# Kernel tuning notes

Hardware: AMD Instinct MI355X
Metric: run time of the kernel (lower is better)

## Reference

```python
import jax, jax.numpy as jnp
import numpy as np

GREEDY_EPS = 1e-6

def setup_inputs() -> dict:
    key = jax.random.key(0)
    k1, k2, k3 = jax.random.split(key, 3)
    B, V = 256, 128000
    logits = jax.random.normal(k1, (B, V), dtype=jnp.float32)
    temperatures = jax.random.uniform(k2, (B,), dtype=jnp.float32)  # in (0,1); some rows near 0 -> greedy-ish
    u = jax.random.uniform(k3, (B, V), dtype=jnp.float32, minval=1e-10, maxval=1.0)
    return {"logits": logits, "temperatures": temperatures, "u": u}

def reference(logits, temperatures, u):
    # Greedy token per row
    greedy = jnp.argmax(logits, axis=-1)  # [B]
    # Temperature-scaled logits; guard temp<=eps rows against div-by-zero
    safe_t = jnp.where(temperatures <= GREEDY_EPS, 1.0, temperatures)  # [B]
    scaled = logits / safe_t[:, None]  # [B, V]
    # Gumbel-max trick: argmax(scaled + g), g ~ Gumbel(0,1), equals
    # multinomial sample from softmax(scaled) in distribution.
    gumbel = -jnp.log(-jnp.log(u))  # [B, V]
    sampled = jnp.argmax(scaled + gumbel, axis=-1)  # [B]
    # Per-row greedy fallback for temp <= eps (matches the torch loop)
    return jnp.where(temperatures <= GREEDY_EPS, greedy, sampled)
```

## Files before the change

### kernel.cpp

```cpp
#include <hip/hip_runtime.h>
#include <math.h>

#define GREEDY_EPS 1e-6f
#define SEG 4
#define BLK 1024

typedef float f32x4 __attribute__((ext_vector_type(4)));

__device__ inline unsigned int fkey(float v) {
    unsigned int b = __float_as_uint(v);
    return (b & 0x80000000u) ? ~b : (b | 0x80000000u);
}

__global__ __launch_bounds__(BLK) void sampler_partial(
    const float* __restrict__ logits,
    const float* __restrict__ temps,
    const float* __restrict__ u,
    unsigned long long* __restrict__ ws,
    int V)
{
    const int row = blockIdx.x >> 2;
    const int seg = blockIdx.x & 3;
    const int tid = threadIdx.x;

    const int segLen = V / SEG;
    const int segOff = seg * segLen;
    const int nvec   = segLen >> 2;

    const float t = temps[row];
    const bool greedy = (t <= GREEDY_EPS);

    const f32x4* __restrict__ lg4 =
        (const f32x4*)(logits + (size_t)row * (size_t)V + segOff);
    const f32x4* __restrict__ uu4 =
        (const f32x4*)(u + (size_t)row * (size_t)V + segOff);

    float bestVal = -INFINITY;
    int bestIdx = 0;

    if (greedy) {
        for (int i = tid; i < nvec; i += BLK) {
            f32x4 l = lg4[i];
            int base = i << 2;
            if (l.x > bestVal) { bestVal = l.x; bestIdx = base; }
            if (l.y > bestVal) { bestVal = l.y; bestIdx = base + 1; }
            if (l.z > bestVal) { bestVal = l.z; bestIdx = base + 2; }
            if (l.w > bestVal) { bestVal = l.w; bestIdx = base + 3; }
        }
    } else {
        const float a   = -t * 0.69314718055994530942f;
        const float ac1 = a * -0.52876637294489770425f;
        for (int i = tid; i < nvec; i += BLK) {
            f32x4 l = lg4[i];
            f32x4 g = __builtin_nontemporal_load(&uu4[i]);
            int base = i << 2;
            float G0 = __log2f(-__log2f(g.x));
            float G1 = __log2f(-__log2f(g.y));
            float G2 = __log2f(-__log2f(g.z));
            float G3 = __log2f(-__log2f(g.w));
            float v0 = fmaf(a, G0, l.x + ac1);
            float v1 = fmaf(a, G1, l.y + ac1);
            float v2 = fmaf(a, G2, l.z + ac1);
            float v3 = fmaf(a, G3, l.w + ac1);
            if (v0 > bestVal) { bestVal = v0; bestIdx = base; }
            if (v1 > bestVal) { bestVal = v1; bestIdx = base + 1; }
            if (v2 > bestVal) { bestVal = v2; bestIdx = base + 2; }
            if (v3 > bestVal) { bestVal = v3; bestIdx = base + 3; }
        }
    }

    const int lane = tid & 63;
    const int wave = tid >> 6;
    #pragma unroll
    for (int off = 32; off > 0; off >>= 1) {
        float ov = __shfl_down(bestVal, off);
        int   oi = __shfl_down(bestIdx, off);
        if (ov > bestVal || (ov == bestVal && oi < bestIdx)) {
            bestVal = ov; bestIdx = oi;
        }
    }

    __shared__ float sVal[BLK / 64];
    __shared__ int   sIdx[BLK / 64];
    if (lane == 0) { sVal[wave] = bestVal; sIdx[wave] = bestIdx; }
    __syncthreads();

    if (tid == 0) {
        float bv = sVal[0]; int bi = sIdx[0];
        #pragma unroll
        for (int w = 1; w < BLK / 64; ++w) {
            float v = sVal[w]; int ix = sIdx[w];
            if (v > bv || (v == bv && ix < bi)) { bv = v; bi = ix; }
        }
        int gidx = bi + segOff;
        unsigned long long packed =
            ((unsigned long long)fkey(bv) << 32) |
            (unsigned long long)(0xFFFFFFFFu - (unsigned int)gidx);
        ws[(size_t)row * SEG + seg] = packed;
    }
}

__global__ void sampler_final(const unsigned long long* __restrict__ ws,
                              int* __restrict__ out, int B)
{
    int row = blockIdx.x * blockDim.x + threadIdx.x;
    if (row < B) {
        unsigned long long m = ws[(size_t)row * SEG];
        #pragma unroll
        for (int s = 1; s < SEG; ++s) {
            unsigned long long v = ws[(size_t)row * SEG + s];
            if (v > m) m = v;
        }
        out[row] = (int)(0xFFFFFFFFu - (unsigned int)(m & 0xFFFFFFFFu));
    }
}

extern "C" void kernel_launch(void* const* d_in, const int* in_sizes, int n_in,
                              void* d_out, int out_size, void* d_ws, size_t ws_size,
                              hipStream_t stream) {
    const float* logits = (const float*)d_in[0];
    const float* temps  = (const float*)d_in[1];
    const float* u      = (const float*)d_in[2];
    int* out = (int*)d_out;

    const int B = in_sizes[1];
    const int V = in_sizes[0] / B;

    unsigned long long* ws = (unsigned long long*)d_ws;

    sampler_partial<<<dim3(B * SEG), dim3(BLK), 0, stream>>>(
        logits, temps, u, ws, V);
    sampler_final<<<dim3((B + 255) / 256), dim3(256), 0, stream>>>(ws, out, B);
}
```

Baseline: 45.87 us.

## Fuse final reduction into partial kernel via atomics and retune segments

Replaces the separate final-reduction kernel with per-row 64-bit atomicMax plus an arrival counter, so the last-arriving block for each row writes the output. Work is split into 8 segments of 512 threads instead of 4 segments of 1024, and the main loops get an unroll-4 hint. This removes one kernel launch but adds a memset of the workspace before every call and atomic traffic. The memset still adds a stream operation, so part of the launch overhead remains.

Result: slower. 135.1 us (+194.6%).

```diff
diff --git a/kernel.cpp b/kernel.cpp
--- a/kernel.cpp
+++ b/kernel.cpp
@@ -2,8 +2,8 @@
 #include <math.h>
 
 #define GREEDY_EPS 1e-6f
-#define SEG 4
-#define BLK 1024
+#define SEG 8
+#define BLK 512
 
 typedef float f32x4 __attribute__((ext_vector_type(4)));
 
@@ -12,15 +12,17 @@
     return (b & 0x80000000u) ? ~b : (b | 0x80000000u);
 }
 
-__global__ __launch_bounds__(BLK) void sampler_partial(
+__global__ __launch_bounds__(BLK) void sampler_fused(
     const float* __restrict__ logits,
     const float* __restrict__ temps,
     const float* __restrict__ u,
-    unsigned long long* __restrict__ ws,
+    unsigned long long* __restrict__ wsMax,
+    unsigned int* __restrict__ wsCnt,
+    int* __restrict__ out,
     int V)
 {
-    const int row = blockIdx.x >> 2;
-    const int seg = blockIdx.x & 3;
+    const int row = blockIdx.x >> 3;
+    const int seg = blockIdx.x & 7;
     const int tid = threadIdx.x;
 
     const int segLen = V / SEG;
@@ -39,6 +41,7 @@
     int bestIdx = 0;
 
     if (greedy) {
+        #pragma unroll 4
         for (int i = tid; i < nvec; i += BLK) {
             f32x4 l = lg4[i];
             int base = i << 2;
@@ -50,6 +53,7 @@
     } else {
         const float a   = -t * 0.69314718055994530942f;
         const float ac1 = a * -0.52876637294489770425f;
+        #pragma unroll 4
         for (int i = tid; i < nvec; i += BLK) {
             f32x4 l = lg4[i];
             f32x4 g = __builtin_nontemporal_load(&uu4[i]);
@@ -96,22 +100,14 @@
         unsigned long long packed =
             ((unsigned long long)fkey(bv) << 32) |
             (unsigned long long)(0xFFFFFFFFu - (unsigned int)gidx);
-        ws[(size_t)row * SEG + seg] = packed;
-    }
-}
 
-__global__ void sampler_final(const unsigned long long* __restrict__ ws,
-                              int* __restrict__ out, int B)
-{
-    int row = blockIdx.x * blockDim.x + threadIdx.x;
-    if (row < B) {
-        unsigned long long m = ws[(size_t)row * SEG];
-        #pragma unroll
-        for (int s = 1; s < SEG; ++s) {
-            unsigned long long v = ws[(size_t)row * SEG + s];
-            if (v > m) m = v;
+        atomicMax(&wsMax[row], packed);
+        __threadfence();
+        unsigned int prev = atomicAdd(&wsCnt[row], 1u);
+        if (prev == SEG - 1) {
+            unsigned long long m = atomicMax(&wsMax[row], 0ULL);
+            out[row] = (int)(0xFFFFFFFFu - (unsigned int)(m & 0xFFFFFFFFu));
         }
-        out[row] = (int)(0xFFFFFFFFu - (unsigned int)(m & 0xFFFFFFFFu));
     }
 }
 
@@ -126,9 +122,11 @@
     const int B = in_sizes[1];
     const int V = in_sizes[0] / B;
 
-    unsigned long long* ws = (unsigned long long*)d_ws;
+    unsigned long long* wsMax = (unsigned long long*)d_ws;
+    unsigned int* wsCnt = (unsigned int*)((char*)d_ws + (size_t)B * 8);
 
-    sampler_partial<<<dim3(B * SEG), dim3(BLK), 0, stream>>>(
-        logits, temps, u, ws, V);
-    sampler_final<<<dim3((B + 255) / 256), dim3(256), 0, stream>>>(ws, out, B);
+    hipMemsetAsync(d_ws, 0, (size_t)B * 12, stream);
+
+    sampler_fused<<<dim3(B * SEG), dim3(BLK), 0, stream>>>(
+        logits, temps, u, wsMax, wsCnt, out, V);
 }
```
